# Performance work log

Measured on AMD Instinct MI355X. Metric: run time of the kernel, lower is better.

Reference implementation:

```python
import jax, jax.numpy as jnp
import numpy as np

N_NODES = 50000
N_EDGES = 800000
C = 128
NEG_SLOPE = 0.01  # nn.LeakyReLU default


def _init_linear(key, fan_in, fan_out):
    kw, kb = jax.random.split(key)
    lim = 1.0 / np.sqrt(fan_in)
    W = jax.random.uniform(kw, (fan_in, fan_out), jnp.float32, -lim, lim)
    b = jax.random.uniform(kb, (fan_out,), jnp.float32, -lim, lim)
    return W, b


def setup_inputs() -> dict:
    key = jax.random.key(0)
    ks = jax.random.split(key, 10)
    x = jax.random.normal(ks[0], (N_NODES, C), jnp.float32)
    pos = jax.random.normal(ks[1], (N_NODES, 3), jnp.float32)
    edge_index = jax.random.randint(ks[2], (2, N_EDGES), 0, N_NODES, jnp.int64)
    # mlp_h: Linear(C,C) -> LeakyReLU -> Linear(C,3) -> Tanh
    Wh1, bh1 = _init_linear(ks[3], C, C)
    Wh2, bh2 = _init_linear(ks[4], C, 3)
    # mlp_f: Linear(C+3, C) -> LeakyReLU
    Wf, bf = _init_linear(ks[5], C + 3, C)
    # mlp_g: Linear(C,C) -> LeakyReLU -> Linear(C,C)
    Wg1, bg1 = _init_linear(ks[6], C, C)
    Wg2, bg2 = _init_linear(ks[7], C, C)
    return {"x": x, "pos": pos, "edge_index": edge_index,
            "Wh1": Wh1, "bh1": bh1, "Wh2": Wh2, "bh2": bh2,
            "Wf": Wf, "bf": bf,
            "Wg1": Wg1, "bg1": bg1, "Wg2": Wg2, "bg2": bg2}


def reference(x, pos, edge_index, Wh1, bh1, Wh2, bh2, Wf, bf, Wg1, bg1, Wg2, bg2):
    lrelu = lambda t: jax.nn.leaky_relu(t, NEG_SLOPE)
    # delta_i = tanh(mlp_h(x_i))  -> [N, 3]
    delta = jnp.tanh(lrelu(x @ Wh1 + bh1) @ Wh2 + bh2)
    src, dst = edge_index[0], edge_index[1]  # message j -> i (PyG convention)
    # per-edge relative position: pos_j - pos_i + delta_i  -> [E, 3]
    rel = pos[src] - pos[dst] + delta[dst]
    # per-edge message: mlp_f([rel, x_j])  -> [E, C]
    e = lrelu(jnp.concatenate([rel, x[src]], axis=-1) @ Wf + bf)
    # scatter-max aggregate over incoming edges per target node
    agg = jax.ops.segment_max(e, dst, num_segments=N_NODES)
    agg = jnp.where(jnp.isfinite(agg), agg, 0.0)  # empty segments -> 0
    # out_i = mlp_g(agg_i) + x_i
    out = lrelu(agg @ Wg1 + bg1) @ Wg2 + bg2 + x
    return out
```

## Files before the change

### kernel.cpp

```cpp
#include <hip/hip_runtime.h>
#include <cfloat>
#include <cmath>

#define NEG_SLOPE 0.01f

typedef __attribute__((ext_vector_type(8))) short short8;
typedef __attribute__((ext_vector_type(4))) float f32x4;

__device__ __forceinline__ float lrelu(float v) { return v >= 0.0f ? v : NEG_SLOPE * v; }

__device__ __forceinline__ ushort f2b(float f) {
    unsigned u = __float_as_uint(f);
    u += 0x7fffu + ((u >> 16) & 1u);
    return (ushort)(u >> 16);
}
__device__ __forceinline__ float b2f(ushort s) { return __uint_as_float(((unsigned)s) << 16); }

__device__ __forceinline__ void split8(const float* v, short8& hi, short8& lo) {
#pragma unroll
    for (int j = 0; j < 8; ++j) {
        ushort h = f2b(v[j]);
        hi[j] = (short)h;
        lo[j] = (short)f2b(v[j] - b2f(h));
    }
}

__global__ __launch_bounds__(256) void count_wprep_kernel(
    const int* __restrict__ ei, int* __restrict__ G, int E,
    const float* __restrict__ Wh1, const float* __restrict__ Wf,
    const float* __restrict__ Wg1, const float* __restrict__ Wg2,
    ushort* __restrict__ WT)
{
    __shared__ int cnt[256];
    const int t = threadIdx.x;
    const int b = blockIdx.x;

    {
        int tt = b * 256 + t;
        int mat = tt >> 14;
        int idx = tt & 16383;
        int n = idx >> 7, k = idx & 127;
        float v;
        if (mat == 0)      v = Wh1[k * 128 + n];
        else if (mat == 1) v = Wf[(k + 3) * 128 + n];
        else if (mat == 2) v = Wg1[k * 128 + n];
        else               v = Wg2[k * 128 + n];
        WT[(tt - idx) + n * 128 + k] = f2b(v);
    }

    cnt[t] = 0;
    __syncthreads();
    for (int e = b * 256 + t; e < E; e += 65536)
        atomicAdd(&cnt[ei[E + e] >> 8], 1);
    __syncthreads();
    G[b * 256 + t] = cnt[t];
}


#define GEMM_CORE_REG(ACC, AH, AL)                                              \
    {                                                                           \
        _Pragma("unroll")                                                       \
        for (int ks = 0; ks < 4; ++ks) {                                        \
            _Pragma("unroll")                                                   \
            for (int nt = 0; nt < 8; ++nt) {                                    \
                short8 bfr = *(const short8*)&Bs[(nt * 16 + ln) * 136 + ks * 32 + qd * 8]; \
                ACC[nt] = __builtin_amdgcn_mfma_f32_16x16x32_bf16(AL[ks], bfr, ACC[nt], 0, 0, 0); \
                ACC[nt] = __builtin_amdgcn_mfma_f32_16x16x32_bf16(AH[ks], bfr, ACC[nt], 0, 0, 0); \
            }                                                                   \
        }                                                                       \
    }

#define STAGE_B(WTP)                                                            \
    {                                                                           \
        _Pragma("unroll")                                                       \
        for (int i = 0; i < 8; ++i) {                                           \
            int c = tid + 256 * i;                                              \
            int r = c >> 4, col8 = (c & 15) * 8;                                \
            *(uint4*)&Bs[r * 136 + col8] = *(const uint4*)((WTP) + r * 128 + col8); \
        }                                                                       \
    }

__global__ __launch_bounds__(256) void hy_scanpart_kernel(
    const int* __restrict__ ei, const int* __restrict__ G,
    int* __restrict__ bbase, uint* __restrict__ bpairs, int E, int GB,
    const float* __restrict__ x, const ushort* __restrict__ WT,
    const float* __restrict__ bh1, const float* __restrict__ Wh2,
    const float* __restrict__ bh2, const float* __restrict__ Wf,
    const float* __restrict__ pos, float* __restrict__ q,
    ushort* __restrict__ yb, int M)
{
    __shared__ ushort Bs[128 * 136];
    __shared__ ushort yS[64 * 128];
    const int tid = threadIdx.x;

    if (blockIdx.x >= GB) {
        int* s   = (int*)yS;
        int* cur = ((int*)yS) + 256;
        const int b = blockIdx.x - GB;
        const int t = tid;

        int cs = 0, pp = 0;
        for (int bb = 0; bb < 256; ++bb) {
            int v = G[bb * 256 + t];
            if (bb < b) pp += v;
            cs += v;
        }
        s[t] = cs;
        __syncthreads();
        for (int d = 1; d < 256; d <<= 1) {
            int a = (t >= d) ? s[t - d] : 0;
            __syncthreads();
            s[t] += a;
            __syncthreads();
        }
        int colbase = s[t] - cs;
        cur[t] = colbase + pp;
        if (b == 0) {
            bbase[t] = colbase;
            if (t == 255) bbase[256] = colbase + cs;
        }
        __syncthreads();

        for (int e = b * 256 + t; e < E; e += 65536) {
            int src = ei[e];
            int dst = ei[E + e];
            int p = atomicAdd(&cur[dst >> 8], 1);
            bpairs[p] = (uint)src | ((uint)(dst & 255) << 24);
        }
        return;
    }

    const int w = tid >> 6, L = tid & 63, qd = L >> 4, ln = L & 15;
    const int row0 = blockIdx.x * 64;
    const int arow = row0 + w * 16 + ln;

    short8 ah[4], al[4];
    {
        const float* base = x + (size_t)((arow < M) ? arow : 0) * 128 + qd * 8;
        float vb[8];
#pragma unroll
        for (int ks = 0; ks < 4; ++ks) {
            float4 v0 = make_float4(0.f, 0.f, 0.f, 0.f), v1 = v0;
            if (arow < M) {
                v0 = *(const float4*)(base + ks * 32);
                v1 = *(const float4*)(base + ks * 32 + 4);
            }
            vb[0] = v0.x; vb[1] = v0.y; vb[2] = v0.z; vb[3] = v0.w;
            vb[4] = v1.x; vb[5] = v1.y; vb[6] = v1.z; vb[7] = v1.w;
            split8(vb, ah[ks], al[ks]);
        }
    }

    STAGE_B(WT);
    __syncthreads();
    f32x4 acc1[8];
#pragma unroll
    for (int nt = 0; nt < 8; ++nt) acc1[nt] = (f32x4){0.f, 0.f, 0.f, 0.f};
    GEMM_CORE_REG(acc1, ah, al);
    __syncthreads();

    STAGE_B(WT + 16384);
    __syncthreads();
    f32x4 acc2[8];
#pragma unroll
    for (int nt = 0; nt < 8; ++nt) acc2[nt] = (f32x4){0.f, 0.f, 0.f, 0.f};
    GEMM_CORE_REG(acc2, ah, al);
    __syncthreads();

    float* h1s = (float*)Bs;
#pragma unroll
    for (int nt = 0; nt < 8; ++nt) {
        int n = nt * 16 + ln;
        float bias = bh1[n];
#pragma unroll
        for (int r = 0; r < 4; ++r)
            h1s[(w * 16 + qd * 4 + r) * 132 + n] = lrelu(acc1[nt][r] + bias);
    }
#pragma unroll
    for (int r = 0; r < 4; ++r) {
        int m = w * 16 + qd * 4 + r;
        int gm = row0 + m;
        float p0 = 0.f, p1 = 0.f, p2 = 0.f;
        if (gm < M) { p0 = pos[gm * 3]; p1 = pos[gm * 3 + 1]; p2 = pos[gm * 3 + 2]; }
#pragma unroll
        for (int nt = 0; nt < 8; ++nt) {
            int n = nt * 16 + ln;
            yS[m * 128 + n] = f2b(acc2[nt][r] + p0 * Wf[n] + p1 * Wf[128 + n] + p2 * Wf[256 + n]);
        }
    }
    __syncthreads();

    int row = tid & 63, cc = tid >> 6;
    if (cc < 3 && row0 + row < M) {
        float s = 0.f;
#pragma unroll
        for (int k4 = 0; k4 < 32; ++k4) {
            float4 h = *(const float4*)&h1s[row * 132 + k4 * 4];
            s += h.x * Wh2[(k4 * 4 + 0) * 3 + cc] + h.y * Wh2[(k4 * 4 + 1) * 3 + cc]
               + h.z * Wh2[(k4 * 4 + 2) * 3 + cc] + h.w * Wh2[(k4 * 4 + 3) * 3 + cc];
        }
        q[(row0 + row) * 3 + cc] = tanhf(s + bh2[cc]) - pos[(row0 + row) * 3 + cc];
    }
#pragma unroll
    for (int i = 0; i < 4; ++i) {
        int c = tid + 256 * i;
        int r = c >> 4, col8 = (c & 15) * 8;
        if (row0 + r < M)
            *(uint4*)(yb + (size_t)(row0 + r) * 128 + col8) = *(const uint4*)&yS[r * 128 + col8];
    }
}

__global__ __launch_bounds__(256) void bucket_csr_kernel(
    const uint* __restrict__ bpairs, const int* __restrict__ bbase,
    int* __restrict__ offs, int* __restrict__ srcs, int E, int M, int NBK)
{
    __shared__ int deg[256], scn[256], cur[256];
    const int b = blockIdx.x;
    const int t = threadIdx.x;
    const int base = bbase[b];
    const int end  = bbase[b + 1];
    deg[t] = 0;
    __syncthreads();
    for (int p = base + t; p < end; p += 256)
        atomicAdd(&deg[bpairs[p] >> 24], 1);
    __syncthreads();
    scn[t] = deg[t];
    __syncthreads();
    for (int d = 1; d < 256; d <<= 1) {
        int a = (t >= d) ? scn[t - d] : 0;
        __syncthreads();
        scn[t] += a;
        __syncthreads();
    }
    int excl = scn[t] - deg[t];
    cur[t] = excl;
    int node = b * 256 + t;
    if (node < M) offs[node] = base + excl;
    if (node == M - 1 || (b == NBK - 1 && t == 255)) offs[M] = E;
    __syncthreads();
    for (int p = base + t; p < end; p += 256) {
        uint pk = bpairs[p];
        int qpos = atomicAdd(&cur[pk >> 24], 1);
        srcs[base + qpos] = (int)(pk & 0xFFFFFFu);
    }
}

__global__ __launch_bounds__(256) void agg_kernel(
    const int* __restrict__ offs, const int* __restrict__ srcs,
    const ushort* __restrict__ yb, ushort* __restrict__ aggb, int M)
{
    int wave = threadIdx.x >> 6;
    int lane = threadIdx.x & 63;
    int node = blockIdx.x * 4 + wave;
    if (node >= M) return;
    int o0 = offs[node], o1 = offs[node + 1];
    float a0 = -INFINITY, a1 = -INFINITY;
    const uint* yp = (const uint*)yb;
    int j = o0;
    for (; j + 7 < o1; j += 8) {
        uint u[8];
#pragma unroll
        for (int t = 0; t < 8; ++t)
            u[t] = yp[(size_t)srcs[j + t] * 64 + lane];
#pragma unroll
        for (int t = 0; t < 8; ++t) {
            a0 = fmaxf(a0, __uint_as_float(u[t] << 16));
            a1 = fmaxf(a1, __uint_as_float(u[t] & 0xFFFF0000u));
        }
    }
    for (; j + 3 < o1; j += 4) {
        uint u[4];
#pragma unroll
        for (int t = 0; t < 4; ++t)
            u[t] = yp[(size_t)srcs[j + t] * 64 + lane];
#pragma unroll
        for (int t = 0; t < 4; ++t) {
            a0 = fmaxf(a0, __uint_as_float(u[t] << 16));
            a1 = fmaxf(a1, __uint_as_float(u[t] & 0xFFFF0000u));
        }
    }
    for (; j < o1; ++j) {
        uint u = yp[(size_t)srcs[j] * 64 + lane];
        a0 = fmaxf(a0, __uint_as_float(u << 16));
        a1 = fmaxf(a1, __uint_as_float(u & 0xFFFF0000u));
    }
    uint pk = (__float_as_uint(a0) >> 16) | (__float_as_uint(a1) & 0xFFFF0000u);
    ((uint*)aggb)[(size_t)node * 64 + lane] = pk;
}

__global__ __launch_bounds__(256) void midout_kernel(
    const ushort* __restrict__ aggb, const float* __restrict__ qv,
    const float* __restrict__ Wf, const float* __restrict__ bfv,
    const ushort* __restrict__ Wg1T, const float* __restrict__ bg1,
    const ushort* __restrict__ Wg2T, const float* __restrict__ bg2,
    const float* __restrict__ x, float* __restrict__ out, int M)
{
    __shared__ ushort Bs[128 * 136];
    __shared__ ushort Ms[64 * 136];
    const int tid = threadIdx.x;
    const int w = tid >> 6, L = tid & 63, qd = L >> 4, ln = L & 15;
    const int row0 = blockIdx.x * 64;
    const int arow = row0 + w * 16 + ln;

    short8 ah[4], al[4];
    {
        bool ok = arow < M;
        const ushort* base = aggb + (size_t)(ok ? arow : 0) * 128 + qd * 8;
        float q0 = 0.f, q1 = 0.f, q2 = 0.f;
        if (ok) { q0 = qv[arow * 3]; q1 = qv[arow * 3 + 1]; q2 = qv[arow * 3 + 2]; }
        float vb[8];
#pragma unroll
        for (int ks = 0; ks < 4; ++ks) {
            union { uint4 u; ushort s[8]; } a;
            a.u = ok ? *(const uint4*)(base + ks * 32) : make_uint4(0xFF80FF80u, 0xFF80FF80u, 0xFF80FF80u, 0xFF80FF80u);
#pragma unroll
            for (int j = 0; j < 8; ++j) {
                int k = ks * 32 + qd * 8 + j;
                float dec = 0.f;
                if (a.s[j] != 0xFF80u)
                    dec = lrelu(b2f(a.s[j]) + q0 * Wf[k] + q1 * Wf[128 + k] + q2 * Wf[256 + k] + bfv[k]);
                vb[j] = dec;
            }
            split8(vb, ah[ks], al[ks]);
        }
    }

    STAGE_B(Wg1T);
    __syncthreads();
    f32x4 macc[8];
#pragma unroll
    for (int nt = 0; nt < 8; ++nt) macc[nt] = (f32x4){0.f, 0.f, 0.f, 0.f};
    GEMM_CORE_REG(macc, ah, al);
    __syncthreads();

#pragma unroll
    for (int nt = 0; nt < 8; ++nt) {
        int n = nt * 16 + ln;
        float bias = bg1[n];
#pragma unroll
        for (int r = 0; r < 4; ++r)
            Ms[(w * 16 + qd * 4 + r) * 136 + n] = f2b(lrelu(macc[nt][r] + bias));
    }
    STAGE_B(Wg2T);
    __syncthreads();

    short8 a2[4];
#pragma unroll
    for (int ks = 0; ks < 4; ++ks)
        a2[ks] = *(const short8*)&Ms[(w * 16 + ln) * 136 + ks * 32 + qd * 8];

    f32x4 acc2[8];
#pragma unroll
    for (int nt = 0; nt < 8; ++nt) acc2[nt] = (f32x4){0.f, 0.f, 0.f, 0.f};
#pragma unroll
    for (int ks = 0; ks < 4; ++ks) {
#pragma unroll
        for (int nt = 0; nt < 8; ++nt) {
            short8 bfr = *(const short8*)&Bs[(nt * 16 + ln) * 136 + ks * 32 + qd * 8];
            acc2[nt] = __builtin_amdgcn_mfma_f32_16x16x32_bf16(a2[ks], bfr, acc2[nt], 0, 0, 0);
        }
    }
    __syncthreads();

    float* outS = (float*)Bs;
#pragma unroll
    for (int r = 0; r < 4; ++r) {
        int m = w * 16 + qd * 4 + r;
#pragma unroll
        for (int nt = 0; nt < 8; ++nt)
            outS[m * 132 + nt * 16 + ln] = acc2[nt][r];
    }
    __syncthreads();
#pragma unroll
    for (int i = 0; i < 8; ++i) {
        int c = tid + 256 * i;
        int r = c >> 5, col4 = (c & 31) * 4;
        int gr = row0 + r;
        if (gr < M) {
            float4 o = *(const float4*)&outS[r * 132 + col4];
            float4 bv = *(const float4*)(bg2 + col4);
            float4 xv = *(const float4*)(x + (size_t)gr * 128 + col4);
            o.x += bv.x + xv.x; o.y += bv.y + xv.y;
            o.z += bv.z + xv.z; o.w += bv.w + xv.w;
            *(float4*)(out + (size_t)gr * 128 + col4) = o;
        }
    }
}

extern "C" void kernel_launch(void* const* d_in, const int* in_sizes, int n_in,
                              void* d_out, int out_size, void* d_ws, size_t ws_size,
                              hipStream_t stream)
{
    const float* x   = (const float*)d_in[0];
    const float* pos = (const float*)d_in[1];
    const int*   ei  = (const int*)d_in[2];
    const float* Wh1 = (const float*)d_in[3];
    const float* bh1 = (const float*)d_in[4];
    const float* Wh2 = (const float*)d_in[5];
    const float* bh2 = (const float*)d_in[6];
    const float* Wf  = (const float*)d_in[7];
    const float* bf  = (const float*)d_in[8];
    const float* Wg1 = (const float*)d_in[9];
    const float* bg1 = (const float*)d_in[10];
    const float* Wg2 = (const float*)d_in[11];
    const float* bg2 = (const float*)d_in[12];
    float* out = (float*)d_out;

    const int M = in_sizes[0] / 128;
    const int E = in_sizes[2] / 2;
    const int NBK = (M + 255) >> 8;

    char* ws = (char*)d_ws;
    size_t off = 0;
    auto alloc = [&](size_t bytes) { void* p = ws + off; off += (bytes + 255) & ~255ull; return p; };
    ushort* yb     = (ushort*)alloc((size_t)M * 128 * sizeof(ushort));
    ushort* aggb   = (ushort*)alloc((size_t)M * 128 * sizeof(ushort));
    ushort* WT     = (ushort*)alloc(4 * 16384 * sizeof(ushort));
    float*  q      = (float*)alloc((size_t)M * 3 * sizeof(float));
    int*    offs   = (int*)alloc((size_t)(M + 1) * sizeof(int));
    int*    G      = (int*)alloc(256 * 256 * sizeof(int));
    int*    bbase  = (int*)alloc(257 * sizeof(int));
    uint*   bpairs = (uint*)alloc((size_t)E * sizeof(uint));
    int*    srcs   = (int*)alloc((size_t)E * sizeof(int));

    const int gb = (M + 63) / 64;

    count_wprep_kernel<<<256, 256, 0, stream>>>(ei, G, E, Wh1, Wf, Wg1, Wg2, WT);
    hy_scanpart_kernel<<<gb + 256, 256, 0, stream>>>(
        ei, G, bbase, bpairs, E, gb,
        x, WT, bh1, Wh2, bh2, Wf, pos, q, yb, M);
    bucket_csr_kernel<<<NBK, 256, 0, stream>>>(bpairs, bbase, offs, srcs, E, M, NBK);
    agg_kernel<<<(M + 3) / 4, 256, 0, stream>>>(offs, srcs, yb, aggb, M);
    midout_kernel<<<gb, 256, 0, stream>>>(aggb, q, Wf, bf,
                                          WT + 2 * 16384, bg1,
                                          WT + 3 * 16384, bg2, x, out, M);
}
```

Baseline: 208.2 us.

## Compute delta projection in registers with shuffles and write y directly

The epilogue of the fused node-GEMM kernel no longer stages h1 and y in shared memory. The Linear(C,3) head is now a per-lane partial dot product reduced with cross-lane shuffles, and y is packed into bf16 pairs and stored straight to global memory. This removes a 16 KB shared buffer and two barriers, and launch bounds are raised to 4 blocks per CU to allow higher occupancy. In exchange the global stores are narrower 32-bit writes rather than 128-bit coalesced rows, and the occupancy hint may force register spills.

```diff
diff --git a/kernel.cpp b/kernel.cpp
--- a/kernel.cpp
+++ b/kernel.cpp
@@ -80,7 +80,7 @@
         }                                                                       \
     }
 
-__global__ __launch_bounds__(256) void hy_scanpart_kernel(
+__global__ __launch_bounds__(256, 4) void hy_scanpart_kernel(
     const int* __restrict__ ei, const int* __restrict__ G,
     int* __restrict__ bbase, uint* __restrict__ bpairs, int E, int GB,
     const float* __restrict__ x, const ushort* __restrict__ WT,
@@ -90,12 +90,12 @@
     ushort* __restrict__ yb, int M)
 {
     __shared__ ushort Bs[128 * 136];
-    __shared__ ushort yS[64 * 128];
+    __shared__ int sp[512];
     const int tid = threadIdx.x;
 
     if (blockIdx.x >= GB) {
-        int* s   = (int*)yS;
-        int* cur = ((int*)yS) + 256;
+        int* s   = sp;
+        int* cur = sp + 256;
         const int b = blockIdx.x - GB;
         const int t = tid;
 
@@ -165,48 +165,55 @@
 #pragma unroll
     for (int nt = 0; nt < 8; ++nt) acc2[nt] = (f32x4){0.f, 0.f, 0.f, 0.f};
     GEMM_CORE_REG(acc2, ah, al);
-    __syncthreads();
-
-    float* h1s = (float*)Bs;
+
+    float qa0[4], qa1[4], qa2[4];
+#pragma unroll
+    for (int r = 0; r < 4; ++r) { qa0[r] = 0.f; qa1[r] = 0.f; qa2[r] = 0.f; }
 #pragma unroll
     for (int nt = 0; nt < 8; ++nt) {
-        int n = nt * 16 + ln;
-        float bias = bh1[n];
-#pragma unroll
-        for (int r = 0; r < 4; ++r)
-            h1s[(w * 16 + qd * 4 + r) * 132 + n] = lrelu(acc1[nt][r] + bias);
-    }
+        int nn = nt * 16 + ln;
+        float bias = bh1[nn];
+        float w0 = Wh2[nn * 3], w1 = Wh2[nn * 3 + 1], w2 = Wh2[nn * 3 + 2];
+#pragma unroll
+        for (int r = 0; r < 4; ++r) {
+            float h = lrelu(acc1[nt][r] + bias);
+            qa0[r] += h * w0; qa1[r] += h * w1; qa2[r] += h * w2;
+        }
+    }
+
 #pragma unroll
     for (int r = 0; r < 4; ++r) {
-        int m = w * 16 + qd * 4 + r;
-        int gm = row0 + m;
+        int gm = row0 + w * 16 + qd * 4 + r;
         float p0 = 0.f, p1 = 0.f, p2 = 0.f;
         if (gm < M) { p0 = pos[gm * 3]; p1 = pos[gm * 3 + 1]; p2 = pos[gm * 3 + 2]; }
 #pragma unroll
         for (int nt = 0; nt < 8; ++nt) {
             int n = nt * 16 + ln;
-            yS[m * 128 + n] = f2b(acc2[nt][r] + p0 * Wf[n] + p1 * Wf[128 + n] + p2 * Wf[256 + n]);
-        }
-    }
-    __syncthreads();
-
-    int row = tid & 63, cc = tid >> 6;
-    if (cc < 3 && row0 + row < M) {
-        float s = 0.f;
-#pragma unroll
-        for (int k4 = 0; k4 < 32; ++k4) {
-            float4 h = *(const float4*)&h1s[row * 132 + k4 * 4];
-            s += h.x * Wh2[(k4 * 4 + 0) * 3 + cc] + h.y * Wh2[(k4 * 4 + 1) * 3 + cc]
-               + h.z * Wh2[(k4 * 4 + 2) * 3 + cc] + h.w * Wh2[(k4 * 4 + 3) * 3 + cc];
-        }
-        q[(row0 + row) * 3 + cc] = tanhf(s + bh2[cc]) - pos[(row0 + row) * 3 + cc];
-    }
-#pragma unroll
-    for (int i = 0; i < 4; ++i) {
-        int c = tid + 256 * i;
-        int r = c >> 4, col8 = (c & 15) * 8;
-        if (row0 + r < M)
-            *(uint4*)(yb + (size_t)(row0 + r) * 128 + col8) = *(const uint4*)&yS[r * 128 + col8];
+            float val = acc2[nt][r] + p0 * Wf[n] + p1 * Wf[128 + n] + p2 * Wf[256 + n];
+            float pv = __shfl_xor(val, 1);
+            if (!(ln & 1) && gm < M) {
+                uint u = (uint)f2b(val) | ((uint)f2b(pv) << 16);
+                ((uint*)yb)[(size_t)gm * 64 + nt * 8 + (ln >> 1)] = u;
+            }
+        }
+    }
+
+#pragma unroll
+    for (int r = 0; r < 4; ++r) {
+#pragma unroll
+        for (int d = 1; d < 16; d <<= 1) {
+            qa0[r] += __shfl_xor(qa0[r], d);
+            qa1[r] += __shfl_xor(qa1[r], d);
+            qa2[r] += __shfl_xor(qa2[r], d);
+        }
+    }
+#pragma unroll
+    for (int r = 0; r < 4; ++r) {
+        int gm = row0 + w * 16 + qd * 4 + r;
+        if (ln < 3 && gm < M) {
+            float sv = (ln == 0) ? qa0[r] : (ln == 1) ? qa1[r] : qa2[r];
+            q[gm * 3 + ln] = tanhf(sv + bh2[ln]) - pos[gm * 3 + ln];
+        }
     }
 }
 
```

Measured after the change: 206.8 us (median of 2 runs). Within noise of the previous version (-0.7%).
